# Kernel optimization log

Hardware: AMD Instinct MI355X
Metric: run time of the kernel (lower is better)

The kernel has to match this reference:

```python
import jax, jax.numpy as jnp
import numpy as np

S, B, H = 2048, 32, 1024

def setup_inputs() -> dict:
    key = jax.random.key(0)
    k1, k2, k3, k4, k5 = jax.random.split(key, 5)
    stdv = 1.0 / np.sqrt(2 * H)  # nn.Linear default init scale (approx, uniform in torch)
    return {
        "hidden": jax.random.normal(k1, (1, B, H), dtype=jnp.float32),
        "encoder_outputs": jax.random.normal(k2, (S, B, H), dtype=jnp.float32),
        "W": jax.random.normal(k3, (H, 2 * H), dtype=jnp.float32) * stdv,
        "b": jax.random.normal(k4, (H,), dtype=jnp.float32) * stdv,
        "v": jax.random.normal(k5, (H,), dtype=jnp.float32) * (1.0 / np.sqrt(H)),
    }

def reference(hidden, encoder_outputs, W, b, v):
    # hidden: (1, B, H); encoder_outputs: (S, B, H)
    h = hidden[0]                              # (B, H)
    e = jnp.swapaxes(encoder_outputs, 0, 1)    # (B, S, H)
    Wh, We = W[:, :H], W[:, H:]                # split concat-linear: cat([H_rep, enc]) @ W^T
    # energy = tanh(Linear(cat([H, enc], -1)))  -> (B, S, H)
    pre_h = h @ Wh.T                           # (B, H), broadcast over S (H is repeated per step)
    pre_e = jnp.einsum('bsh,kh->bsk', e, We)   # (B, S, H)
    energy = jnp.tanh(pre_e + pre_h[:, None, :] + b)
    scores = jnp.einsum('bsk,k->bs', energy, v)  # v-dot per position -> (B, S)
    return jax.nn.softmax(scores, axis=1)[:, None, :]  # (B, 1, S)
```

## Files before the change

kernel.cpp:

```cpp
#include <hip/hip_runtime.h>


#define LDT 40

typedef __attribute__((ext_vector_type(8))) short short8;
typedef __attribute__((ext_vector_type(4))) float floatx4;

__device__ __forceinline__ short f2b(float f) {
  union { float f; unsigned u; } c; c.f = f;
  unsigned r = c.u + 0x7fffu + ((c.u >> 16) & 1u);
  return (short)(r >> 16);
}

__device__ __forceinline__ float fast_tanh(float x) {
  float e = __expf(2.0f * x);
  return 1.0f - 2.0f / (e + 1.0f);
}

__global__ __launch_bounds__(256) void k_preh(
    const float* __restrict__ hidden, const float* __restrict__ W,
    const float* __restrict__ bias, float* __restrict__ tpre) {
  const int wv   = (blockIdx.x << 2) + (threadIdx.x >> 6);
  const int lane = threadIdx.x & 63;
  const int b = wv & 31;
  const int k = wv >> 5;
  const float* wr = W + (size_t)k * 2048;
  const float* hr = hidden + b * 1024;
  float s = 0.f;
  #pragma unroll
  for (int j = 0; j < 1024; j += 64) s += wr[j + lane] * hr[j + lane];
  #pragma unroll
  for (int off = 32; off; off >>= 1) s += __shfl_xor(s, off, 64);
  if (lane == 0) tpre[b * 1024 + k] = s + bias[k];
}

__global__ __launch_bounds__(256) void k_gemm(
    const float* __restrict__ A,
    const float* __restrict__ W,
    const float* __restrict__ tpre,
    const float* __restrict__ vvec,
    float* __restrict__ scores) {
  __shared__ short As[128 * LDT];
  __shared__ short Bs[128 * LDT];

  const int l = blockIdx.x;
  const int x = l & 7;
  const int j = l >> 3;
  const int Mbase = (x * 64 + (j >> 3)) * 128;
  const int Nbase = (j & 7) * 128;

  const int tid  = threadIdx.x;
  const int lane = tid & 63;
  const int w    = tid >> 6;
  const int wm   = w >> 1, wn = w & 1;
  const int c    = lane & 15, q = lane >> 4;

  const int tr = tid >> 1;
  const int tc = (tid & 1) * 16;
  const float* ap = A + (size_t)(Mbase + tr) * 1024 + tc;
  const float* bp = W + (size_t)(Nbase + tr) * 2048 + 1024 + tc;
  short* asw = &As[tr * LDT + tc];
  short* bsw = &Bs[tr * LDT + tc];

  floatx4 acc[4][4];
  #pragma unroll
  for (int mt = 0; mt < 4; ++mt)
    #pragma unroll
    for (int nt = 0; nt < 4; ++nt) {
      floatx4 z = {0.f, 0.f, 0.f, 0.f};
      acc[mt][nt] = z;
    }

  for (int k0 = 0; k0 < 1024; k0 += 32) {
    float4 a0 = *(const float4*)(ap + k0);
    float4 a1 = *(const float4*)(ap + k0 + 4);
    float4 a2 = *(const float4*)(ap + k0 + 8);
    float4 a3 = *(const float4*)(ap + k0 + 12);
    float4 b0 = *(const float4*)(bp + k0);
    float4 b1 = *(const float4*)(bp + k0 + 4);
    float4 b2 = *(const float4*)(bp + k0 + 8);
    float4 b3 = *(const float4*)(bp + k0 + 12);
    __syncthreads();
    short8 pa0 = {f2b(a0.x), f2b(a0.y), f2b(a0.z), f2b(a0.w),
                  f2b(a1.x), f2b(a1.y), f2b(a1.z), f2b(a1.w)};
    short8 pa1 = {f2b(a2.x), f2b(a2.y), f2b(a2.z), f2b(a2.w),
                  f2b(a3.x), f2b(a3.y), f2b(a3.z), f2b(a3.w)};
    short8 pb0 = {f2b(b0.x), f2b(b0.y), f2b(b0.z), f2b(b0.w),
                  f2b(b1.x), f2b(b1.y), f2b(b1.z), f2b(b1.w)};
    short8 pb1 = {f2b(b2.x), f2b(b2.y), f2b(b2.z), f2b(b2.w),
                  f2b(b3.x), f2b(b3.y), f2b(b3.z), f2b(b3.w)};
    *(short8*)asw = pa0;
    *(short8*)(asw + 8) = pa1;
    *(short8*)bsw = pb0;
    *(short8*)(bsw + 8) = pb1;
    __syncthreads();

    short8 af[4], bf[4];
    #pragma unroll
    for (int mt = 0; mt < 4; ++mt)
      af[mt] = *(const short8*)&As[(wm * 64 + mt * 16 + c) * LDT + q * 8];
    #pragma unroll
    for (int nt = 0; nt < 4; ++nt)
      bf[nt] = *(const short8*)&Bs[(wn * 64 + nt * 16 + c) * LDT + q * 8];
    #pragma unroll
    for (int mt = 0; mt < 4; ++mt)
      #pragma unroll
      for (int nt = 0; nt < 4; ++nt)
        acc[mt][nt] = __builtin_amdgcn_mfma_f32_16x16x32_bf16(
            af[mt], bf[nt], acc[mt][nt], 0, 0, 0);
  }

  const int mwave = Mbase + wm * 64;
  const int nwave = Nbase + wn * 64;
  float vv[4];
  #pragma unroll
  for (int nt = 0; nt < 4; ++nt) vv[nt] = vvec[nwave + nt * 16 + c];
  #pragma unroll
  for (int mt = 0; mt < 4; ++mt) {
    #pragma unroll
    for (int i = 0; i < 4; ++i) {
      const int mrow = mwave + mt * 16 + q * 4 + i;
      const float* tb = tpre + (mrow & 31) * 1024;
      float ssum = 0.f;
      #pragma unroll
      for (int nt = 0; nt < 4; ++nt) {
        float pre = acc[mt][nt][i] + tb[nwave + nt * 16 + c];
        ssum += fast_tanh(pre) * vv[nt];
      }
      #pragma unroll
      for (int off = 1; off < 16; off <<= 1) ssum += __shfl_xor(ssum, off, 64);
      if (c == 0) atomicAdd(&scores[mrow], ssum);
    }
  }
}

__global__ __launch_bounds__(256) void k_softmax(
    const float* __restrict__ scores, float* __restrict__ out) {
  const int b = blockIdx.x;
  const int t = threadIdx.x;
  const int w = t >> 6, lane = t & 63;
  __shared__ float red[4];
  float vals[8];
  float m = -3.0e38f;
  #pragma unroll
  for (int i = 0; i < 8; ++i) {
    vals[i] = scores[(t + 256 * i) * 32 + b];
    m = fmaxf(m, vals[i]);
  }
  #pragma unroll
  for (int off = 32; off; off >>= 1) m = fmaxf(m, __shfl_xor(m, off, 64));
  if (lane == 0) red[w] = m;
  __syncthreads();
  m = fmaxf(fmaxf(red[0], red[1]), fmaxf(red[2], red[3]));
  __syncthreads();
  float e[8];
  float sum = 0.f;
  #pragma unroll
  for (int i = 0; i < 8; ++i) { e[i] = __expf(vals[i] - m); sum += e[i]; }
  #pragma unroll
  for (int off = 32; off; off >>= 1) sum += __shfl_xor(sum, off, 64);
  if (lane == 0) red[w] = sum;
  __syncthreads();
  sum = red[0] + red[1] + red[2] + red[3];
  const float inv = 1.0f / sum;
  #pragma unroll
  for (int i = 0; i < 8; ++i) out[b * 2048 + t + 256 * i] = e[i] * inv;
}

extern "C" void kernel_launch(void* const* d_in, const int* in_sizes, int n_in,
                              void* d_out, int out_size, void* d_ws, size_t ws_size,
                              hipStream_t stream) {
  const float* hidden = (const float*)d_in[0];
  const float* enc    = (const float*)d_in[1];
  const float* W      = (const float*)d_in[2];
  const float* bias   = (const float*)d_in[3];
  const float* vvec   = (const float*)d_in[4];
  float* out = (float*)d_out;

  float* scores = (float*)d_ws;
  float* tpre   = scores + 65536;

  hipMemsetAsync(scores, 0, 65536 * sizeof(float), stream);
  hipLaunchKernelGGL(k_preh, dim3(8192), dim3(256), 0, stream, hidden, W, bias, tpre);
  hipLaunchKernelGGL(k_gemm, dim3(4096), dim3(256), 0, stream, enc, W, tpre, vvec, scores);
  hipLaunchKernelGGL(k_softmax, dim3(32), dim3(256), 0, stream, scores, out);
}
```

Before: 683.2 us.

## Pre-convert W to bf16 and stream B tiles directly into LDS

Adds a kernel that converts the encoder half of W to bf16 once per call. The GEMM then loads B tiles with global_load_lds straight into shared memory, with no per-tile fp32 loads or conversion in registers. The A conversion switches to a perm-based pack (round-half-up rather than round-to-nearest-even), and scores are stored transposed so the softmax reads contiguously. The extra pass over W and the unpadded B tile in LDS may add bank conflicts and launch overhead.

```diff
diff --git a/kernel.cpp b/kernel.cpp
--- a/kernel.cpp
+++ b/kernel.cpp
@@ -5,16 +5,37 @@
 
 typedef __attribute__((ext_vector_type(8))) short short8;
 typedef __attribute__((ext_vector_type(4))) float floatx4;
-
-__device__ __forceinline__ short f2b(float f) {
+typedef __attribute__((ext_vector_type(4))) unsigned int uint4v;
+
+#define GLDS(g, l) __builtin_amdgcn_global_load_lds( \
+    (const __attribute__((address_space(1))) void*)(g), \
+    (__attribute__((address_space(3))) void*)(l), 16, 0, 0)
+
+__device__ __forceinline__ unsigned short f2b(float f) {
   union { float f; unsigned u; } c; c.f = f;
   unsigned r = c.u + 0x7fffu + ((c.u >> 16) & 1u);
-  return (short)(r >> 16);
+  return (unsigned short)(r >> 16);
+}
+
+__device__ __forceinline__ unsigned pack2(float lo, float hi) {
+  union { float f; unsigned u; } a, b; a.f = lo; b.f = hi;
+  return __builtin_amdgcn_perm(b.u + 0x8000u, a.u + 0x8000u, 0x07060302u);
 }
 
 __device__ __forceinline__ float fast_tanh(float x) {
   float e = __expf(2.0f * x);
   return 1.0f - 2.0f / (e + 1.0f);
+}
+
+__global__ __launch_bounds__(256) void k_cvtB(
+    const float* __restrict__ W, unsigned int* __restrict__ Bw) {
+  const int idx = blockIdx.x * 256 + threadIdx.x;
+  const int row = idx >> 8, col = (idx & 255) << 2;
+  float4 f = *(const float4*)(W + (size_t)row * 2048 + 1024 + col);
+  unsigned u0 = (unsigned)f2b(f.x) | ((unsigned)f2b(f.y) << 16);
+  unsigned u1 = (unsigned)f2b(f.z) | ((unsigned)f2b(f.w) << 16);
+  uint2 u = {u0, u1};
+  *(uint2*)(Bw + ((size_t)row * 1024 + col) / 2) = u;
 }
 
 __global__ __launch_bounds__(256) void k_preh(
@@ -36,31 +57,30 @@
 
 __global__ __launch_bounds__(256) void k_gemm(
     const float* __restrict__ A,
-    const float* __restrict__ W,
+    const unsigned short* __restrict__ Bw,
     const float* __restrict__ tpre,
     const float* __restrict__ vvec,
-    float* __restrict__ scores) {
+    float* __restrict__ scoresT) {
   __shared__ short As[128 * LDT];
-  __shared__ short Bs[128 * LDT];
+  __shared__ short Bs[128 * 32];
 
   const int l = blockIdx.x;
-  const int x = l & 7;
-  const int j = l >> 3;
+  const int x = l & 7, j = l >> 3;
   const int Mbase = (x * 64 + (j >> 3)) * 128;
   const int Nbase = (j & 7) * 128;
 
-  const int tid  = threadIdx.x;
-  const int lane = tid & 63;
-  const int w    = tid >> 6;
-  const int wm   = w >> 1, wn = w & 1;
-  const int c    = lane & 15, q = lane >> 4;
-
-  const int tr = tid >> 1;
-  const int tc = (tid & 1) * 16;
-  const float* ap = A + (size_t)(Mbase + tr) * 1024 + tc;
-  const float* bp = W + (size_t)(Nbase + tr) * 2048 + 1024 + tc;
-  short* asw = &As[tr * LDT + tc];
-  short* bsw = &Bs[tr * LDT + tc];
+  const int tid = threadIdx.x, lane = tid & 63, w = tid >> 6;
+  const int wm = w >> 1, wn = w & 1;
+  const int c = lane & 15, q = lane >> 4;
+
+  const float* ap = A + (size_t)(Mbase + (tid >> 1)) * 1024 + ((tid & 1) << 4);
+  short* asw = &As[(tid >> 1) * LDT + ((tid & 1) << 4)];
+
+  const unsigned short* bg0 =
+      Bw + (size_t)(Nbase + w * 32 + (lane >> 2)) * 1024 + ((lane & 3) << 3);
+  const unsigned short* bg1 = bg0 + (size_t)16 * 1024;
+  short* bl0 = &Bs[(w * 32) * 32];
+  short* bl1 = &Bs[(w * 32 + 16) * 32];
 
   floatx4 acc[4][4];
   #pragma unroll
@@ -72,27 +92,19 @@
     }
 
   for (int k0 = 0; k0 < 1024; k0 += 32) {
-    float4 a0 = *(const float4*)(ap + k0);
-    float4 a1 = *(const float4*)(ap + k0 + 4);
-    float4 a2 = *(const float4*)(ap + k0 + 8);
-    float4 a3 = *(const float4*)(ap + k0 + 12);
-    float4 b0 = *(const float4*)(bp + k0);
-    float4 b1 = *(const float4*)(bp + k0 + 4);
-    float4 b2 = *(const float4*)(bp + k0 + 8);
-    float4 b3 = *(const float4*)(bp + k0 + 12);
+    float4 f0 = *(const float4*)(ap + k0);
+    float4 f1 = *(const float4*)(ap + k0 + 4);
+    float4 f2 = *(const float4*)(ap + k0 + 8);
+    float4 f3 = *(const float4*)(ap + k0 + 12);
     __syncthreads();
-    short8 pa0 = {f2b(a0.x), f2b(a0.y), f2b(a0.z), f2b(a0.w),
-                  f2b(a1.x), f2b(a1.y), f2b(a1.z), f2b(a1.w)};
-    short8 pa1 = {f2b(a2.x), f2b(a2.y), f2b(a2.z), f2b(a2.w),
-                  f2b(a3.x), f2b(a3.y), f2b(a3.z), f2b(a3.w)};
-    short8 pb0 = {f2b(b0.x), f2b(b0.y), f2b(b0.z), f2b(b0.w),
-                  f2b(b1.x), f2b(b1.y), f2b(b1.z), f2b(b1.w)};
-    short8 pb1 = {f2b(b2.x), f2b(b2.y), f2b(b2.z), f2b(b2.w),
-                  f2b(b3.x), f2b(b3.y), f2b(b3.z), f2b(b3.w)};
-    *(short8*)asw = pa0;
-    *(short8*)(asw + 8) = pa1;
-    *(short8*)bsw = pb0;
-    *(short8*)(bsw + 8) = pb1;
+    GLDS(bg0 + k0, bl0);
+    GLDS(bg1 + k0, bl1);
+    uint4v u0 = {pack2(f0.x, f0.y), pack2(f0.z, f0.w),
+                 pack2(f1.x, f1.y), pack2(f1.z, f1.w)};
+    uint4v u1 = {pack2(f2.x, f2.y), pack2(f2.z, f2.w),
+                 pack2(f3.x, f3.y), pack2(f3.z, f3.w)};
+    *(uint4v*)asw = u0;
+    *(uint4v*)(asw + 8) = u1;
     __syncthreads();
 
     short8 af[4], bf[4];
@@ -101,7 +113,7 @@
       af[mt] = *(const short8*)&As[(wm * 64 + mt * 16 + c) * LDT + q * 8];
     #pragma unroll
     for (int nt = 0; nt < 4; ++nt)
-      bf[nt] = *(const short8*)&Bs[(wn * 64 + nt * 16 + c) * LDT + q * 8];
+      bf[nt] = *(const short8*)&Bs[(wn * 64 + nt * 16 + c) * 32 + q * 8];
     #pragma unroll
     for (int mt = 0; mt < 4; ++mt)
       #pragma unroll
@@ -129,13 +141,13 @@
       }
       #pragma unroll
       for (int off = 1; off < 16; off <<= 1) ssum += __shfl_xor(ssum, off, 64);
-      if (c == 0) atomicAdd(&scores[mrow], ssum);
+      if (c == 0) atomicAdd(&scoresT[(mrow & 31) * 2048 + (mrow >> 5)], ssum);
     }
   }
 }
 
 __global__ __launch_bounds__(256) void k_softmax(
-    const float* __restrict__ scores, float* __restrict__ out) {
+    const float* __restrict__ scoresT, float* __restrict__ out) {
   const int b = blockIdx.x;
   const int t = threadIdx.x;
   const int w = t >> 6, lane = t & 63;
@@ -144,7 +156,7 @@
   float m = -3.0e38f;
   #pragma unroll
   for (int i = 0; i < 8; ++i) {
-    vals[i] = scores[(t + 256 * i) * 32 + b];
+    vals[i] = scoresT[b * 2048 + t + 256 * i];
     m = fmaxf(m, vals[i]);
   }
   #pragma unroll
@@ -177,11 +189,14 @@
   const float* vvec   = (const float*)d_in[4];
   float* out = (float*)d_out;
 
-  float* scores = (float*)d_ws;
-  float* tpre   = scores + 65536;
-
-  hipMemsetAsync(scores, 0, 65536 * sizeof(float), stream);
+  float* scoresT = (float*)d_ws;
+  float* tpre    = scoresT + 65536;
+  unsigned int* Bw = (unsigned int*)(tpre + 32768);
+
+  hipMemsetAsync(scoresT, 0, 65536 * sizeof(float), stream);
+  hipLaunchKernelGGL(k_cvtB, dim3(1024), dim3(256), 0, stream, W, Bw);
   hipLaunchKernelGGL(k_preh, dim3(8192), dim3(256), 0, stream, hidden, W, bias, tpre);
-  hipLaunchKernelGGL(k_gemm, dim3(4096), dim3(256), 0, stream, enc, W, tpre, vvec, scores);
-  hipLaunchKernelGGL(k_softmax, dim3(32), dim3(256), 0, stream, scores, out);
-}
+  hipLaunchKernelGGL(k_gemm, dim3(4096), dim3(256), 0, stream,
+                     enc, (const unsigned short*)Bw, tpre, vvec, scoresT);
+  hipLaunchKernelGGL(k_softmax, dim3(32), dim3(256), 0, stream, scoresT, out);
+}
```

Result: slower. 719.5 us (+5.3%).
